# Optimization experiments

Measured on AMD Instinct MI355X. Metric: run time of the kernel, lower is better.

## Reference

```python
import jax, jax.numpy as jnp
import numpy as np

N_SRC = 30000
N_DST = 30000
D = 256        # in_channels == out_channels (required for the original code to run)
R = 8          # num_relations
E = 300000     # num edges


def setup_inputs() -> dict:
    key = jax.random.key(0)
    ks = jax.random.split(key, 10)
    s = 0.05  # weight scale
    return {
        "x_src": jax.random.normal(ks[0], (N_SRC, D), jnp.float32),
        "x_dst": jax.random.normal(ks[1], (N_DST, D), jnp.float32),
        "edge_index": jax.random.randint(ks[2], (2, E), 0, N_DST, dtype=jnp.int64),
        "edge_type": jax.random.randint(ks[3], (E,), 0, R, dtype=jnp.int64),
        "w1": jax.random.normal(ks[4], (R, D, D), jnp.float32) * s,
        "root1": jax.random.normal(ks[5], (D, D), jnp.float32) * s,
        "b1": jnp.zeros((D,), jnp.float32),
        "w2": jax.random.normal(ks[6], (R, D, D), jnp.float32) * s,
        "root2": jax.random.normal(ks[7], (D, D), jnp.float32) * s,
        "b2": jnp.zeros((D,), jnp.float32),
    }


def _rgcn_conv(x_src, x_dst, src, dst, etype, W, root, bias):
    """PyG RGCNConv (aggr='mean', root_weight=True) on bipartite (x_src, x_dst).
    Per relation r: mean-aggregate x_src over edges of type r into dst, then @ W[r].
    """
    n_dst, d = x_dst.shape[0], x_src.shape[1]
    # fuse (dst, relation) into one segment id -> single gather + single scatter
    seg = dst * R + etype                                   # (E,)
    msgs = x_src[src]                                       # (E, d) gather
    sums = jax.ops.segment_sum(msgs, seg, num_segments=n_dst * R)
    sums = sums.reshape(n_dst, R, d)                        # (Nd, R, d)
    cnt = jax.ops.segment_sum(jnp.ones((seg.shape[0],), x_src.dtype), seg,
                              num_segments=n_dst * R).reshape(n_dst, R, 1)
    agg = sums / jnp.maximum(cnt, 1.0)                      # mean aggregation
    out = jnp.einsum('nrd,rde->ne', agg, W)                 # per-relation transform
    out = out + x_dst @ root + bias                         # root + bias
    return out


def reference(x_src, x_dst, edge_index, edge_type, w1, root1, b1, w2, root2, b2):
    src, dst = edge_index[0], edge_index[1]
    h = jax.nn.relu(_rgcn_conv(x_src, x_dst, src, dst, edge_type, w1, root1, b1))
    out = _rgcn_conv(x_src, h, src, dst, edge_type, w2, root2, b2)
    # new_x_dict['src'] is identically zero in the original; return dst output
    return out
```

## Files before the change

kernel.cpp:

```cpp
#include <hip/hip_runtime.h>
#include <hip/hip_bf16.h>

#define D_DIM 256
#define R_REL 8
#define KT 2304

typedef __attribute__((ext_vector_type(8))) short short8;
typedef __attribute__((ext_vector_type(4))) float f32x4;

static __device__ __forceinline__ unsigned short f2bf(float f) {
  unsigned u = __float_as_uint(f);
  u += 0x7FFF + ((u >> 16) & 1);
  return (unsigned short)(u >> 16);
}


__global__ void k_build_bt(const float* __restrict__ w, const float* __restrict__ root,
                           unsigned short* __restrict__ bt) {
  int idx = blockIdx.x * 256 + threadIdx.x;
  if (idx >= D_DIM * KT) return;
  int n = idx / KT, k = idx - n * KT;
  float v = (k < R_REL * D_DIM) ? w[(size_t)k * D_DIM + n]
                                : root[(size_t)(k - R_REL * D_DIM) * D_DIM + n];
  bt[idx] = f2bf(v);
}

__global__ void k_cvt_bf16(const float* __restrict__ in, unsigned short* __restrict__ out,
                           int n4) {
  int i = blockIdx.x * 256 + threadIdx.x;
  if (i >= n4) return;
  float4 v = ((const float4*)in)[i];
  ushort4 o = { f2bf(v.x), f2bf(v.y), f2bf(v.z), f2bf(v.w) };
  ((ushort4*)out)[i] = o;
}


__global__ void k_link(const int* __restrict__ dst, const int* __restrict__ et,
                       int* __restrict__ head, int* __restrict__ nxt, int E) {
  int e = blockIdx.x * 256 + threadIdx.x;
  if (e >= E) return;
  int seg = dst[e] * R_REL + et[e];
  nxt[e] = atomicExch(&head[seg], e);
}

__global__ void k_gather(const float* __restrict__ xsrc, const int* __restrict__ src,
                         const int* __restrict__ nxt, const int* __restrict__ head,
                         unsigned short* __restrict__ agg, int seg0, int nsegc) {
  int sg = blockIdx.x * 4 + (threadIdx.x >> 6);
  if (sg >= nsegc) return;
  int lane = threadIdx.x & 63;
  int e = head[seg0 + sg];
  float4 acc = {0.f, 0.f, 0.f, 0.f};
  int n = 0;
  while (e >= 0) {
    int s = src[e];
    float4 v = ((const float4*)(xsrc + (size_t)s * D_DIM))[lane];
    acc.x += v.x; acc.y += v.y; acc.z += v.z; acc.w += v.w;
    ++n;
    e = nxt[e];
  }
  float inv = (n > 0) ? (1.0f / (float)n) : 0.0f;
  ushort4 o = { f2bf(acc.x * inv), f2bf(acc.y * inv), f2bf(acc.z * inv), f2bf(acc.w * inv) };
  ((ushort4*)(agg + (size_t)sg * 256))[lane] = o;
}


__device__ __forceinline__ void gload_lds16(const void* g, void* l) {
  __builtin_amdgcn_global_load_lds(
      (const __attribute__((address_space(1))) void*)g,
      (__attribute__((address_space(3))) void*)l, 16, 0, 0);
}

__global__ __launch_bounds__(512, 2) void k_fused(
    const unsigned short* __restrict__ Agg,
    const unsigned short* __restrict__ Xd,
    const unsigned short* __restrict__ Bt1,
    const unsigned short* __restrict__ Bt2,
    const float* __restrict__ b1,
    const float* __restrict__ b2,
    float* __restrict__ Out,
    int M) {
  extern __shared__ __align__(16) char lds[];
  char* smA  = lds;
  char* smB1 = lds + 16 * 1024;
  char* smB2 = lds + 48 * 1024;
  char* smH  = lds + 80 * 1024;

  int tid = threadIdx.x;
  int bm = blockIdx.x;
  int lane = tid & 63;
  int wid = tid >> 6;
  int wm = wid >> 2, wn = wid & 3;
  int lr = lane & 15, lk = lane >> 4;

  f32x4 acc1[4][4] = {};
  f32x4 acc2[4][4] = {};

  int arow = tid >> 2, aslot = tid & 3;

  auto stageA = [&](int buf, int step) {
    const unsigned short* Ap; int strideA, colA;
    if (step < 64) { Ap = Agg; strideA = 2048; colA = step * 32; }
    else           { Ap = Xd;  strideA = 256;  colA = (step - 64) * 32; }
    int gr = bm * 128 + arow; if (gr >= M) gr = M - 1;
    int srcslot = aslot ^ ((arow >> 1) & 3);
    gload_lds16(Ap + (size_t)gr * strideA + colA + srcslot * 8,
                smA + buf * 8192 + tid * 16);
  };
  auto stageB = [&](char* smB, int buf, const unsigned short* Bt, int kcol) {
#pragma unroll
    for (int i = 0; i < 2; ++i) {
      int u = i * 512 + tid;
      int row = u >> 2, slot = u & 3;
      int srcslot = slot ^ ((row >> 1) & 3);
      gload_lds16(Bt + (size_t)row * KT + kcol + srcslot * 8,
                  smB + buf * 16384 + u * 16);
    }
  };

  stageA(0, 0); stageB(smB1, 0, Bt1, 0); stageB(smB2, 0, Bt2, 0);
  asm volatile("s_waitcnt vmcnt(0)" ::: "memory");
  __syncthreads();

  int buf = 0;
  for (int t = 0; t < 64; ++t) {
    stageA(buf ^ 1, t + 1);
    stageB(smB1, buf ^ 1, Bt1, (t + 1) * 32);
    if (t + 1 < 64) stageB(smB2, buf ^ 1, Bt2, (t + 1) * 32);
    short8 af[4], bfr1[4], bfr2[4];
#pragma unroll
    for (int m = 0; m < 4; ++m) {
      int row = wm * 64 + m * 16 + lr;
      af[m] = *(const short8*)(smA + buf * 8192 + row * 64 + ((lk ^ ((row >> 1) & 3)) << 4));
    }
#pragma unroll
    for (int n = 0; n < 4; ++n) {
      int row = wn * 64 + n * 16 + lr;
      int off = row * 64 + ((lk ^ ((row >> 1) & 3)) << 4);
      bfr1[n] = *(const short8*)(smB1 + buf * 16384 + off);
      bfr2[n] = *(const short8*)(smB2 + buf * 16384 + off);
    }
#pragma unroll
    for (int m = 0; m < 4; ++m)
#pragma unroll
      for (int n = 0; n < 4; ++n) {
        acc1[m][n] = __builtin_amdgcn_mfma_f32_16x16x32_bf16(af[m], bfr1[n], acc1[m][n], 0, 0, 0);
        acc2[m][n] = __builtin_amdgcn_mfma_f32_16x16x32_bf16(af[m], bfr2[n], acc2[m][n], 0, 0, 0);
      }
    asm volatile("s_waitcnt vmcnt(0)" ::: "memory");
    __syncthreads();
    buf ^= 1;
  }

  for (int t = 64; t < 72; ++t) {
    if (t < 71) {
      stageA(buf ^ 1, t + 1);
      stageB(smB1, buf ^ 1, Bt1, (t + 1) * 32);
    }
    short8 af[4], bfr1[4];
#pragma unroll
    for (int m = 0; m < 4; ++m) {
      int row = wm * 64 + m * 16 + lr;
      af[m] = *(const short8*)(smA + buf * 8192 + row * 64 + ((lk ^ ((row >> 1) & 3)) << 4));
    }
#pragma unroll
    for (int n = 0; n < 4; ++n) {
      int row = wn * 64 + n * 16 + lr;
      bfr1[n] = *(const short8*)(smB1 + buf * 16384 + row * 64 + ((lk ^ ((row >> 1) & 3)) << 4));
    }
#pragma unroll
    for (int m = 0; m < 4; ++m)
#pragma unroll
      for (int n = 0; n < 4; ++n)
        acc1[m][n] = __builtin_amdgcn_mfma_f32_16x16x32_bf16(af[m], bfr1[n], acc1[m][n], 0, 0, 0);
    asm volatile("s_waitcnt vmcnt(0)" ::: "memory");
    __syncthreads();
    buf ^= 1;
  }

  float b1v[4];
#pragma unroll
  for (int n = 0; n < 4; ++n) b1v[n] = b1[wn * 64 + n * 16 + lr];
#pragma unroll
  for (int m = 0; m < 4; ++m)
#pragma unroll
    for (int n = 0; n < 4; ++n)
#pragma unroll
      for (int j = 0; j < 4; ++j) {
        int row = wm * 64 + m * 16 + lk * 4 + j;
        int col = wn * 64 + n * 16 + lr;
        float v = fmaxf(acc1[m][n][j] + b1v[n], 0.0f);
        *(unsigned short*)(smH + row * 512 + ((col * 2) ^ ((row & 7) << 4))) = f2bf(v);
      }
  __syncthreads();

  stageB(smB2, 0, Bt2, 2048);
  asm volatile("s_waitcnt vmcnt(0)" ::: "memory");
  __syncthreads();
  for (int s = 0; s < 8; ++s) {
    if (s < 7) stageB(smB2, (s + 1) & 1, Bt2, 2048 + (s + 1) * 32);
    short8 ah[4], bfr2[4];
#pragma unroll
    for (int m = 0; m < 4; ++m) {
      int row = wm * 64 + m * 16 + lr;
      ah[m] = *(const short8*)(smH + row * 512 + ((s * 64 + lk * 16) ^ ((row & 7) << 4)));
    }
#pragma unroll
    for (int n = 0; n < 4; ++n) {
      int row = wn * 64 + n * 16 + lr;
      bfr2[n] = *(const short8*)(smB2 + (s & 1) * 16384 + row * 64 + ((lk ^ ((row >> 1) & 3)) << 4));
    }
#pragma unroll
    for (int m = 0; m < 4; ++m)
#pragma unroll
      for (int n = 0; n < 4; ++n)
        acc2[m][n] = __builtin_amdgcn_mfma_f32_16x16x32_bf16(ah[m], bfr2[n], acc2[m][n], 0, 0, 0);
    asm volatile("s_waitcnt vmcnt(0)" ::: "memory");
    __syncthreads();
  }

  float b2v[4];
#pragma unroll
  for (int n = 0; n < 4; ++n) b2v[n] = b2[wn * 64 + n * 16 + lr];
#pragma unroll
  for (int m = 0; m < 4; ++m)
#pragma unroll
    for (int n = 0; n < 4; ++n)
#pragma unroll
      for (int j = 0; j < 4; ++j) {
        int row = bm * 128 + wm * 64 + m * 16 + lk * 4 + j;
        if (row < M)
          Out[(size_t)row * D_DIM + wn * 64 + n * 16 + lr] = acc2[m][n][j] + b2v[n];
      }
}


extern "C" void kernel_launch(void* const* d_in, const int* in_sizes, int n_in,
                              void* d_out, int out_size, void* d_ws, size_t ws_size,
                              hipStream_t stream) {
  const float* x_src = (const float*)d_in[0];
  const float* x_dst = (const float*)d_in[1];
  const int*   eidx  = (const int*)d_in[2];
  const int*   etype = (const int*)d_in[3];
  const float* w1    = (const float*)d_in[4];
  const float* root1 = (const float*)d_in[5];
  const float* b1    = (const float*)d_in[6];
  const float* w2    = (const float*)d_in[7];
  const float* root2 = (const float*)d_in[8];
  const float* b2    = (const float*)d_in[9];

  const int E  = in_sizes[3];
  const int Nd = in_sizes[1] / D_DIM;
  const int nseg = Nd * R_REL;
  const int* srcI = eidx;
  const int* dstI = eidx + E;

  char* ws = (char*)d_ws;
  size_t off = 0;
  auto alloc = [&](size_t bytes) {
    size_t o = off;
    off += (bytes + 255) & ~(size_t)255;
    return o;
  };
  size_t o_bt1  = alloc((size_t)D_DIM * KT * 2);
  size_t o_bt2  = alloc((size_t)D_DIM * KT * 2);
  size_t o_xd   = alloc((size_t)Nd * D_DIM * 2);
  size_t o_head = alloc((size_t)nseg * 4);
  size_t o_nxt  = alloc((size_t)E * 4);
  size_t fixed_end = off;

  const size_t per_node = 4096;
  long long avail = (long long)ws_size - (long long)fixed_end - 4096;
  int Nc = avail > 0 ? (int)(avail / (long long)per_node) : 0;
  if (Nc > Nd) Nc = Nd;
  Nc = (Nc / 128) * 128;
  if (Nc < 128) {
    hipMemsetAsync(d_out, 0, (size_t)out_size * 4, stream);
    return;
  }
  int nchunks = (Nd + Nc - 1) / Nc;
  int NcB = (((Nd + nchunks - 1) / nchunks) + 127) / 128 * 128;
  if (NcB <= Nc) Nc = NcB;
  nchunks = (Nd + Nc - 1) / Nc;

  unsigned short* bt1  = (unsigned short*)(ws + o_bt1);
  unsigned short* bt2  = (unsigned short*)(ws + o_bt2);
  unsigned short* xd16 = (unsigned short*)(ws + o_xd);
  int* head = (int*)(ws + o_head);
  int* nxt  = (int*)(ws + o_nxt);
  unsigned short* agg_c = (unsigned short*)(ws + fixed_end);

  const int LDS_BYTES = 144 * 1024;
  hipFuncSetAttribute((const void*)k_fused,
                      hipFuncAttributeMaxDynamicSharedMemorySize, LDS_BYTES);

  hipMemsetAsync(head, 0xFF, (size_t)nseg * 4, stream);
  k_build_bt<<<(D_DIM * KT + 255) / 256, 256, 0, stream>>>(w1, root1, bt1);
  k_build_bt<<<(D_DIM * KT + 255) / 256, 256, 0, stream>>>(w2, root2, bt2);
  k_cvt_bf16<<<(Nd * 64 + 255) / 256, 256, 0, stream>>>(x_dst, xd16, Nd * 64);
  k_link<<<(E + 255) / 256, 256, 0, stream>>>(dstI, etype, head, nxt, E);

  for (int c = 0; c < nchunks; ++c) {
    int n0 = c * Nc;
    int Mc = Nd - n0 < Nc ? Nd - n0 : Nc;
    int nsegc = Mc * R_REL;
    k_gather<<<(nsegc + 3) / 4, 256, 0, stream>>>(x_src, srcI, nxt, head,
                                                  agg_c, n0 * R_REL, nsegc);
    int mb = (Mc + 127) / 128;
    k_fused<<<mb, 512, LDS_BYTES, stream>>>(agg_c, xd16 + (size_t)n0 * D_DIM,
                                            bt1, bt2, b1, b2,
                                            (float*)d_out + (size_t)n0 * D_DIM, Mc);
  }
}
```

Measured before the change: 369.0 us.

## Triple-buffer fused GEMM pipeline with partial vmcnt waits and larger gather blocks

The fused two-layer GEMM kernel moves from double buffering, with a full vmcnt(0) drain every k-step, to a three-stage LDS ring. Each step prefetches two stages ahead and waits only until the current stage's loads have landed, so global-to-LDS loads overlap the MFMA work. Waits use raw s_barrier plus counted vmcnt and are retuned for the tail phases. The gather kernel now runs 16 segments per 1024-thread block, and chunk sizing no longer rounds to 128-row multiples. The cost is more LDS ring space overlapping the H staging area and tighter hand-managed synchronisation that must stay correct.

New measurement: 303.4 us. -17.8%, faster.

```diff
diff --git a/kernel.cpp b/kernel.cpp
--- a/kernel.cpp
+++ b/kernel.cpp
@@ -7,6 +7,8 @@
 
 typedef __attribute__((ext_vector_type(8))) short short8;
 typedef __attribute__((ext_vector_type(4))) float f32x4;
+
+#define WAITCNT_VM(N) asm volatile("s_waitcnt vmcnt(" #N ")" ::: "memory")
 
 static __device__ __forceinline__ unsigned short f2bf(float f) {
   unsigned u = __float_as_uint(f);
@@ -46,7 +48,7 @@
 __global__ void k_gather(const float* __restrict__ xsrc, const int* __restrict__ src,
                          const int* __restrict__ nxt, const int* __restrict__ head,
                          unsigned short* __restrict__ agg, int seg0, int nsegc) {
-  int sg = blockIdx.x * 4 + (threadIdx.x >> 6);
+  int sg = blockIdx.x * 16 + (threadIdx.x >> 6);
   if (sg >= nsegc) return;
   int lane = threadIdx.x & 63;
   int e = head[seg0 + sg];
@@ -81,10 +83,7 @@
     float* __restrict__ Out,
     int M) {
   extern __shared__ __align__(16) char lds[];
-  char* smA  = lds;
-  char* smB1 = lds + 16 * 1024;
-  char* smB2 = lds + 48 * 1024;
-  char* smH  = lds + 80 * 1024;
+  char* smH = lds + 80 * 1024;
 
   int tid = threadIdx.x;
   int bm = blockIdx.x;
@@ -97,87 +96,126 @@
   f32x4 acc2[4][4] = {};
 
   int arow = tid >> 2, aslot = tid & 3;
-
-  auto stageA = [&](int buf, int step) {
+  int gr = bm * 128 + arow; if (gr >= M) gr = M - 1;
+
+  auto stageA = [&](int set, int step) {
     const unsigned short* Ap; int strideA, colA;
     if (step < 64) { Ap = Agg; strideA = 2048; colA = step * 32; }
     else           { Ap = Xd;  strideA = 256;  colA = (step - 64) * 32; }
-    int gr = bm * 128 + arow; if (gr >= M) gr = M - 1;
     int srcslot = aslot ^ ((arow >> 1) & 3);
     gload_lds16(Ap + (size_t)gr * strideA + colA + srcslot * 8,
-                smA + buf * 8192 + tid * 16);
-  };
-  auto stageB = [&](char* smB, int buf, const unsigned short* Bt, int kcol) {
+                lds + set * 40960 + tid * 16);
+  };
+  auto stageB = [&](int set, int bsel , int kcol) {
+    const unsigned short* Bt = bsel ? Bt2 : Bt1;
 #pragma unroll
     for (int i = 0; i < 2; ++i) {
       int u = i * 512 + tid;
       int row = u >> 2, slot = u & 3;
       int srcslot = slot ^ ((row >> 1) & 3);
       gload_lds16(Bt + (size_t)row * KT + kcol + srcslot * 8,
-                  smB + buf * 16384 + u * 16);
-    }
-  };
-
-  stageA(0, 0); stageB(smB1, 0, Bt1, 0); stageB(smB2, 0, Bt2, 0);
-  asm volatile("s_waitcnt vmcnt(0)" ::: "memory");
-  __syncthreads();
-
-  int buf = 0;
-  for (int t = 0; t < 64; ++t) {
-    stageA(buf ^ 1, t + 1);
-    stageB(smB1, buf ^ 1, Bt1, (t + 1) * 32);
-    if (t + 1 < 64) stageB(smB2, buf ^ 1, Bt2, (t + 1) * 32);
-    short8 af[4], bfr1[4], bfr2[4];
+                  lds + set * 40960 + 8192 + bsel * 16384 + u * 16);
+    }
+  };
+  auto stage_full = [&](int set, int step) {
+    stageA(set, step);
+    stageB(set, 0, step * 32);
+    stageB(set, 1, step * 32);
+  };
+  auto stage_tail = [&](int set, int step) {
+    stageA(set, step);
+    stageB(set, 0, step * 32);
+  };
+  auto stageB2L2 = [&](int half, int kcol) {
+#pragma unroll
+    for (int i = 0; i < 2; ++i) {
+      int u = i * 512 + tid;
+      int row = u >> 2, slot = u & 3;
+      int srcslot = slot ^ ((row >> 1) & 3);
+      gload_lds16(Bt2 + (size_t)row * KT + kcol + srcslot * 8,
+                  lds + half * 16384 + u * 16);
+    }
+  };
+
+  auto loadA = [&](int set, short8* af) {
 #pragma unroll
     for (int m = 0; m < 4; ++m) {
       int row = wm * 64 + m * 16 + lr;
-      af[m] = *(const short8*)(smA + buf * 8192 + row * 64 + ((lk ^ ((row >> 1) & 3)) << 4));
-    }
+      af[m] = *(const short8*)(lds + set * 40960 + row * 64 +
+                               ((lk ^ ((row >> 1) & 3)) << 4));
+    }
+  };
+  auto loadB = [&](int set, int bsel, short8* bf) {
 #pragma unroll
     for (int n = 0; n < 4; ++n) {
       int row = wn * 64 + n * 16 + lr;
-      int off = row * 64 + ((lk ^ ((row >> 1) & 3)) << 4);
-      bfr1[n] = *(const short8*)(smB1 + buf * 16384 + off);
-      bfr2[n] = *(const short8*)(smB2 + buf * 16384 + off);
-    }
+      bf[n] = *(const short8*)(lds + set * 40960 + 8192 + bsel * 16384 +
+                               row * 64 + ((lk ^ ((row >> 1) & 3)) << 4));
+    }
+  };
+
+  stage_full(0, 0);
+  stage_full(1, 1);
+  WAITCNT_VM(5);
+  __builtin_amdgcn_s_barrier();
+
+  for (int t = 0; t < 62; ++t) {
+    stage_full((t + 2) % 3, t + 2);
+    int set = t % 3;
+    short8 af[4], bf1[4], bf2[4];
+    loadA(set, af); loadB(set, 0, bf1); loadB(set, 1, bf2);
 #pragma unroll
     for (int m = 0; m < 4; ++m)
 #pragma unroll
       for (int n = 0; n < 4; ++n) {
-        acc1[m][n] = __builtin_amdgcn_mfma_f32_16x16x32_bf16(af[m], bfr1[n], acc1[m][n], 0, 0, 0);
-        acc2[m][n] = __builtin_amdgcn_mfma_f32_16x16x32_bf16(af[m], bfr2[n], acc2[m][n], 0, 0, 0);
+        acc1[m][n] = __builtin_amdgcn_mfma_f32_16x16x32_bf16(af[m], bf1[n], acc1[m][n], 0, 0, 0);
+        acc2[m][n] = __builtin_amdgcn_mfma_f32_16x16x32_bf16(af[m], bf2[n], acc2[m][n], 0, 0, 0);
       }
-    asm volatile("s_waitcnt vmcnt(0)" ::: "memory");
-    __syncthreads();
-    buf ^= 1;
-  }
-
-  for (int t = 64; t < 72; ++t) {
-    if (t < 71) {
-      stageA(buf ^ 1, t + 1);
-      stageB(smB1, buf ^ 1, Bt1, (t + 1) * 32);
-    }
-    short8 af[4], bfr1[4];
-#pragma unroll
-    for (int m = 0; m < 4; ++m) {
-      int row = wm * 64 + m * 16 + lr;
-      af[m] = *(const short8*)(smA + buf * 8192 + row * 64 + ((lk ^ ((row >> 1) & 3)) << 4));
-    }
-#pragma unroll
-    for (int n = 0; n < 4; ++n) {
-      int row = wn * 64 + n * 16 + lr;
-      bfr1[n] = *(const short8*)(smB1 + buf * 16384 + row * 64 + ((lk ^ ((row >> 1) & 3)) << 4));
-    }
+    WAITCNT_VM(5);
+    __builtin_amdgcn_s_barrier();
+  }
+  for (int t = 62; t < 64; ++t) {
+    stage_tail((t + 2) % 3, t + 2);
+    int set = t % 3;
+    short8 af[4], bf1[4], bf2[4];
+    loadA(set, af); loadB(set, 0, bf1); loadB(set, 1, bf2);
+#pragma unroll
+    for (int m = 0; m < 4; ++m)
+#pragma unroll
+      for (int n = 0; n < 4; ++n) {
+        acc1[m][n] = __builtin_amdgcn_mfma_f32_16x16x32_bf16(af[m], bf1[n], acc1[m][n], 0, 0, 0);
+        acc2[m][n] = __builtin_amdgcn_mfma_f32_16x16x32_bf16(af[m], bf2[n], acc2[m][n], 0, 0, 0);
+      }
+    WAITCNT_VM(3);
+    __builtin_amdgcn_s_barrier();
+  }
+  for (int t = 64; t < 70; ++t) {
+    stage_tail((t + 2) % 3, t + 2);
+    int set = t % 3;
+    short8 af[4], bf1[4];
+    loadA(set, af); loadB(set, 0, bf1);
 #pragma unroll
     for (int m = 0; m < 4; ++m)
 #pragma unroll
       for (int n = 0; n < 4; ++n)
-        acc1[m][n] = __builtin_amdgcn_mfma_f32_16x16x32_bf16(af[m], bfr1[n], acc1[m][n], 0, 0, 0);
-    asm volatile("s_waitcnt vmcnt(0)" ::: "memory");
-    __syncthreads();
-    buf ^= 1;
-  }
-
+        acc1[m][n] = __builtin_amdgcn_mfma_f32_16x16x32_bf16(af[m], bf1[n], acc1[m][n], 0, 0, 0);
+    WAITCNT_VM(3);
+    __builtin_amdgcn_s_barrier();
+  }
+  for (int t = 70; t < 72; ++t) {
+    int set = t % 3;
+    short8 af[4], bf1[4];
+    loadA(set, af); loadB(set, 0, bf1);
+#pragma unroll
+    for (int m = 0; m < 4; ++m)
+#pragma unroll
+      for (int n = 0; n < 4; ++n)
+        acc1[m][n] = __builtin_amdgcn_mfma_f32_16x16x32_bf16(af[m], bf1[n], acc1[m][n], 0, 0, 0);
+    WAITCNT_VM(0);
+    __builtin_amdgcn_s_barrier();
+  }
+
+  stageB2L2(0, 2048);
   float b1v[4];
 #pragma unroll
   for (int n = 0; n < 4; ++n) b1v[n] = b1[wn * 64 + n * 16 + lr];
@@ -192,14 +230,12 @@
         float v = fmaxf(acc1[m][n][j] + b1v[n], 0.0f);
         *(unsigned short*)(smH + row * 512 + ((col * 2) ^ ((row & 7) << 4))) = f2bf(v);
       }
-  __syncthreads();
-
-  stageB(smB2, 0, Bt2, 2048);
-  asm volatile("s_waitcnt vmcnt(0)" ::: "memory");
-  __syncthreads();
+  asm volatile("s_waitcnt vmcnt(0) lgkmcnt(0)" ::: "memory");
+  __builtin_amdgcn_s_barrier();
+
   for (int s = 0; s < 8; ++s) {
-    if (s < 7) stageB(smB2, (s + 1) & 1, Bt2, 2048 + (s + 1) * 32);
-    short8 ah[4], bfr2[4];
+    if (s < 7) stageB2L2((s + 1) & 1, 2048 + (s + 1) * 32);
+    short8 ah[4], bf2[4];
 #pragma unroll
     for (int m = 0; m < 4; ++m) {
       int row = wm * 64 + m * 16 + lr;
@@ -208,15 +244,16 @@
 #pragma unroll
     for (int n = 0; n < 4; ++n) {
       int row = wn * 64 + n * 16 + lr;
-      bfr2[n] = *(const short8*)(smB2 + (s & 1) * 16384 + row * 64 + ((lk ^ ((row >> 1) & 3)) << 4));
+      bf2[n] = *(const short8*)(lds + ((s & 1) * 16384) + row * 64 +
+                                ((lk ^ ((row >> 1) & 3)) << 4));
     }
 #pragma unroll
     for (int m = 0; m < 4; ++m)
 #pragma unroll
       for (int n = 0; n < 4; ++n)
-        acc2[m][n] = __builtin_amdgcn_mfma_f32_16x16x32_bf16(ah[m], bfr2[n], acc2[m][n], 0, 0, 0);
-    asm volatile("s_waitcnt vmcnt(0)" ::: "memory");
-    __syncthreads();
+        acc2[m][n] = __builtin_amdgcn_mfma_f32_16x16x32_bf16(ah[m], bf2[n], acc2[m][n], 0, 0, 0);
+    WAITCNT_VM(0);
+    __builtin_amdgcn_s_barrier();
   }
 
   float b2v[4];
@@ -273,15 +310,11 @@
   long long avail = (long long)ws_size - (long long)fixed_end - 4096;
   int Nc = avail > 0 ? (int)(avail / (long long)per_node) : 0;
   if (Nc > Nd) Nc = Nd;
-  Nc = (Nc / 128) * 128;
-  if (Nc < 128) {
+  if (Nc < 1) {
     hipMemsetAsync(d_out, 0, (size_t)out_size * 4, stream);
     return;
   }
   int nchunks = (Nd + Nc - 1) / Nc;
-  int NcB = (((Nd + nchunks - 1) / nchunks) + 127) / 128 * 128;
-  if (NcB <= Nc) Nc = NcB;
-  nchunks = (Nd + Nc - 1) / Nc;
 
   unsigned short* bt1  = (unsigned short*)(ws + o_bt1);
   unsigned short* bt2  = (unsigned short*)(ws + o_bt2);
@@ -304,8 +337,8 @@
     int n0 = c * Nc;
     int Mc = Nd - n0 < Nc ? Nd - n0 : Nc;
     int nsegc = Mc * R_REL;
-    k_gather<<<(nsegc + 3) / 4, 256, 0, stream>>>(x_src, srcI, nxt, head,
-                                                  agg_c, n0 * R_REL, nsegc);
+    k_gather<<<(nsegc + 15) / 16, 1024, 0, stream>>>(x_src, srcI, nxt, head,
+                                                     agg_c, n0 * R_REL, nsegc);
     int mb = (Mc + 127) / 128;
     k_fused<<<mb, 512, LDS_BYTES, stream>>>(agg_c, xd16 + (size_t)n0 * D_DIM,
                                             bt1, bt2, b1, b2,
```
